# Performance work log

Measured on AMD Instinct MI355X. Metric: run time of the kernel, lower is better.

Reference implementation:

```python
import jax, jax.numpy as jnp
import numpy as np

# RPE constants from the source: pix_per_patch=200//16, alpha=12, beta=24, gamma=96, num_buckets=49
ALPHA, BETA, GAMMA, PPP = 12.0, 24.0, 96.0, 12.0
NUM_BUCKETS = 49
LN_EPS = 1e-5


def _layernorm(x, w, b):
    m = jnp.mean(x, axis=-1, keepdims=True)
    v = jnp.mean((x - m) ** 2, axis=-1, keepdims=True)
    return (x - m) / jnp.sqrt(v + LN_EPS) * w + b


def _bucket_ids(ct):
    # ct: (B,T,2) int coords -> piecewise_index bucket ids shifted by beta, (B,T,T) int32
    ctf = ct.astype(jnp.float32)
    diff = ctf[:, :, None, :] - ctf[:, None, :, :]          # (B,T,T,2)
    dist = jnp.sqrt(jnp.sum(diff * diff, axis=-1))           # euclidean distance
    rel = jnp.trunc(dist / PPP)                              # torch.div(..., rounding_mode='trunc')
    abs_r = jnp.abs(rel)
    log_branch = jnp.sign(rel) * jnp.minimum(
        jnp.round(ALPHA + jnp.log(jnp.maximum(abs_r, 1e-6) / ALPHA) / np.log(GAMMA / ALPHA) * (BETA - ALPHA)),
        BETA)
    idx = jnp.where(abs_r <= ALPHA, jnp.round(rel), log_branch).astype(jnp.int32)
    return idx + int(BETA)                                   # shift into [0, num_buckets)


def setup_inputs() -> dict:
    key = jax.random.key(0)
    ks = jax.random.split(key, 12)
    B, T, C, H = 32, 500, 512, 8
    s = 0.02
    return {
        "x": jax.random.normal(ks[0], (B, T, C), jnp.float32),
        "ct": jax.random.randint(ks[1], (B, T, 2), 0, 200, jnp.int32),
        "w_attn": jax.random.normal(ks[2], (C, 3 * C), jnp.float32) * s,
        "b_attn": jnp.zeros((3 * C,), jnp.float32),
        "w_proj": jax.random.normal(ks[3], (C, C), jnp.float32) * s,
        "b_proj": jnp.zeros((C,), jnp.float32),
        "rpe_table": jax.random.normal(ks[4], (H, NUM_BUCKETS), jnp.float32) * s,
        "ln1_w": jnp.ones((C,), jnp.float32),
        "ln1_b": jnp.zeros((C,), jnp.float32),
        "ln2_w": jnp.ones((C,), jnp.float32),
        "ln2_b": jnp.zeros((C,), jnp.float32),
        "w_fc": jax.random.normal(ks[5], (C, 2 * C), jnp.float32) * s,
        "b_fc": jnp.zeros((2 * C,), jnp.float32),
        "w_fc2": jax.random.normal(ks[6], (2 * C, C), jnp.float32) * s,
        "b_fc2": jnp.zeros((C,), jnp.float32),
    }


def reference(x, ct, w_attn, b_attn, w_proj, b_proj, rpe_table,
              ln1_w, ln1_b, ln2_w, ln2_b, w_fc, b_fc, w_fc2, b_fc2):
    B, T, C = x.shape
    H = rpe_table.shape[0]
    D = C // H

    # --- RPEAttention ---
    bucket = _bucket_ids(ct)                                  # (B,T,T) int32 in [0,49)
    qkv = x @ w_attn + b_attn                                 # (B,T,3C)
    q, k, v = jnp.split(qkv, 3, axis=-1)
    q = q.reshape(B, T, H, D).transpose(0, 2, 1, 3)           # (B,H,T,D)
    k = k.reshape(B, T, H, D).transpose(0, 2, 1, 3)
    v = v.reshape(B, T, H, D).transpose(0, 2, 1, 3)
    att = jnp.einsum('bhtd,bhsd->bhts', q, k) * (1.0 / np.sqrt(D))
    # bias buffer is all ones -> masked_fill(bias==0) is a no-op
    # faithful replication of torch: table[:, flat].view(B,H,T,T) (a raw reshape of (H, B*T*T))
    rpe = rpe_table[:, bucket.reshape(-1)].reshape(B, H, T, T)
    att = jax.nn.softmax(att + rpe, axis=-1)
    y = jnp.einsum('bhts,bhsd->bthd', att, v).reshape(B, T, C)
    y = y @ w_proj + b_proj

    # --- Block: residual + LN, MLP (GELU exact), residual + LN ---
    x = _layernorm(x + y, ln1_w, ln1_b)
    h = jax.nn.gelu(x @ w_fc + b_fc, approximate=False)
    x = _layernorm(x + (h @ w_fc2 + b_fc2), ln2_w, ln2_b)
    return x
```

## Files before the change

### kernel.cpp

```cpp
#include <hip/hip_runtime.h>
#include <cstdint>
#include <cstddef>


typedef unsigned short ushort_t;
typedef __bf16 bf16x8 __attribute__((ext_vector_type(8)));
typedef float floatx4 __attribute__((ext_vector_type(4)));
typedef unsigned short ushort4v __attribute__((ext_vector_type(4)));
typedef unsigned short ushort8v __attribute__((ext_vector_type(8)));

#define DEV __device__ __forceinline__

#define B_ 32
#define T_ 500
#define C_ 512
#define H_ 8
#define M_ 16000

#define OFF_QK     0ULL
#define OFF_XBF    32800768ULL
#define OFF_BUCKET 49184768ULL
#define OFF_VT     57376768ULL
#define OFF_Y      74153984ULL
#define OFF_WATTN  90537984ULL
#define OFF_WPROJ  92110848ULL
#define OFF_WFC    92635136ULL
#define OFF_WFC2   93683712ULL
#define VT_BYTES   16777216ULL

DEV ushort_t f2bf(float f) {
  union { float f; unsigned u; } v; v.f = f;
  unsigned r = v.u + 0x7fffu + ((v.u >> 16) & 1u);
  return (ushort_t)(r >> 16);
}
DEV float bf2f(ushort_t u) {
  union { unsigned u; float f; } v; v.u = ((unsigned)u) << 16;
  return v.f;
}

DEV void gload16(const void* g, void* l) {
  __builtin_amdgcn_global_load_lds(
      (__attribute__((address_space(1))) void*)(g),
      (__attribute__((address_space(3))) void*)(l), 16, 0, 0);
}

__global__ __launch_bounds__(256) void cvt_bf16(const float* __restrict__ in,
                                                ushort_t* __restrict__ out, int n) {
  int i = (blockIdx.x * 256 + threadIdx.x) * 4;
  if (i >= n) return;
  float4 v = *(const float4*)(in + i);
  ushort4v o = { f2bf(v.x), f2bf(v.y), f2bf(v.z), f2bf(v.w) };
  *(ushort4v*)(out + i) = o;
}

struct WTDesc { const float* w; ushort_t* wt; int K; int N; };
struct WTArgs { WTDesc d[4]; };

__global__ __launch_bounds__(256) void wtrans_all(WTArgs a) {
  const int bid = blockIdx.x;
  int z, local;
  if (bid < 768)       { z = 0; local = bid; }
  else if (bid < 1024) { z = 1; local = bid - 768; }
  else if (bid < 1536) { z = 2; local = bid - 1024; }
  else                 { z = 3; local = bid - 1536; }
  const WTDesc dd = a.d[z];
  const int gx = dd.N >> 5;
  const int n0 = (local % gx) * 32, k0 = (local / gx) * 32;

  __shared__ float tile[32][33];
  const int c = threadIdx.x & 31, r = threadIdx.x >> 5;
#pragma unroll
  for (int rr = 0; rr < 4; ++rr)
    tile[r + rr * 8][c] = dd.w[(size_t)(k0 + r + rr * 8) * dd.N + n0 + c];
  __syncthreads();
#pragma unroll
  for (int rr = 0; rr < 4; ++rr)
    dd.wt[(size_t)(n0 + r + rr * 8) * dd.K + k0 + c] = f2bf(tile[c][r + rr * 8]);
}

__global__ __launch_bounds__(256) void bucket_kernel(const int* __restrict__ ct,
                                                     unsigned char* __restrict__ bucket) {
  const int b = blockIdx.y;
  const int tid = threadIdx.x, w = tid >> 6, lane = tid & 63;
  __shared__ int2 ctS[500];
  for (int j = tid; j < T_; j += 256) ctS[j] = ((const int2*)ct)[(size_t)b * T_ + j];
  __syncthreads();
  const int t = blockIdx.x * 4 + w;
  const int2 a = ctS[t];
  const float ax = (float)a.x, ay = (float)a.y;
  const size_t rowbase = (size_t)(b * T_ + t) << 9;
#pragma unroll
  for (int it = 0; it < 8; ++it) {
    const int s = it * 64 + lane;
    if (s < T_) {
      const int2 c2 = ctS[s];
      const float dx = ax - (float)c2.x, dy = ay - (float)c2.y;
      const float dist = sqrtf(dx * dx + dy * dy);
      const float rel = truncf(dist / 12.0f);
      const float far = fminf(rintf(12.0f + logf(rel / 12.0f) * (12.0f / 2.0794415416798357f)), 24.0f);
      const float idx = (rel <= 12.0f) ? rel : far;
      bucket[rowbase + (s >> 6) * 64 + (s & 15) * 4 + ((s >> 4) & 3)]
          = (unsigned char)((int)idx + 24);
    }
  }
}

__global__ __launch_bounds__(256, 2)
void gemm_qkv(const ushort_t* __restrict__ A,
              const ushort_t* __restrict__ Bt,
              const float* __restrict__ bias,
              ushort_t* __restrict__ qk,
              ushort_t* __restrict__ vt) {
  constexpr int K = 512;
  const int bid = blockIdx.x;
  const int xcd = bid & 7, k = bid >> 3;
  const int n_blk = k % 12, mg = k / 12;
  const int m_blk = mg * 8 + xcd;
  if (m_blk >= 125) return;
  const int m0 = m_blk * 128, n0 = n_blk * 128;

  __shared__ __align__(16) ushort_t As[128 * 64];
  __shared__ __align__(16) ushort_t Bs[128 * 64];
  const int tid = threadIdx.x;
  const int lane = tid & 63, w = tid >> 6;
  const int wm = w >> 1, wn = w & 1;
  const int quad = lane >> 4, l15 = lane & 15;

  floatx4 acc[4][4] = {};

  for (int k0 = 0; k0 < K; k0 += 64) {
    __syncthreads();
#pragma unroll
    for (int j = 0; j < 4; ++j) {
      const int chunk = j * 256 + tid;
      const int row = chunk >> 3, pos = chunk & 7, c = pos ^ (row & 7);
      gload16(A + (size_t)(m0 + row) * K + k0 + c * 8, (char*)As + j * 4096 + w * 1024);
      gload16(Bt + (size_t)(n0 + row) * K + k0 + c * 8, (char*)Bs + j * 4096 + w * 1024);
    }
    asm volatile("s_waitcnt vmcnt(0)" ::: "memory");
    __syncthreads();

#pragma unroll
    for (int kq = 0; kq < 2; ++kq) {
      bf16x8 af[4], bfr[4];
#pragma unroll
      for (int t = 0; t < 4; ++t) {
        const int rowa = wm * 64 + t * 16 + l15;
        const int posa = (kq * 4 + quad) ^ (rowa & 7);
        af[t] = *(const bf16x8*)((const char*)As + rowa * 128 + posa * 16);
        const int rowb = wn * 64 + t * 16 + l15;
        const int posb = (kq * 4 + quad) ^ (rowb & 7);
        bfr[t] = *(const bf16x8*)((const char*)Bs + rowb * 128 + posb * 16);
      }
#pragma unroll
      for (int tm = 0; tm < 4; ++tm)
#pragma unroll
        for (int tn = 0; tn < 4; ++tn)
          acc[tm][tn] = __builtin_amdgcn_mfma_f32_16x16x32_bf16(af[tm], bfr[tn], acc[tm][tn], 0, 0, 0);
    }
  }

  if (n0 < 1024) {
#pragma unroll
    for (int tn = 0; tn < 4; ++tn) {
      const int n = n0 + wn * 64 + tn * 16 + l15;
      const float bs = bias[n];
#pragma unroll
      for (int tm = 0; tm < 4; ++tm)
#pragma unroll
        for (int r = 0; r < 4; ++r) {
          const int m = m0 + wm * 64 + tm * 16 + quad * 4 + r;
          qk[(size_t)m * 1024 + n] = f2bf(acc[tm][tn][r] + bs);
        }
    }
  } else {
#pragma unroll
    for (int tn = 0; tn < 4; ++tn) {
      const int n = n0 + wn * 64 + tn * 16 + l15;
      const float bs = bias[n];
      const int hh = (n >> 6) - 16, dd = n & 63;
#pragma unroll
      for (int tm = 0; tm < 4; ++tm) {
        const int mb = m0 + wm * 64 + tm * 16 + quad * 4;
        const int bb = mb / 500;
        const int ss = mb - bb * 500;
        ushort4v pk;
#pragma unroll
        for (int r = 0; r < 4; ++r) pk[r] = f2bf(acc[tm][tn][r] + bs);
        *(ushort4v*)(vt + (((size_t)(bb * 8 + hh)) * 64 + dd) * 512 + ss) = pk;
      }
    }
  }
}

template <int TN, int EPI>
__global__ __launch_bounds__(256, TN == 64 ? 4 : 2)
void gemm_bt(const ushort_t* __restrict__ A,
             const ushort_t* __restrict__ Bt,
             const float* __restrict__ bias,
             const float* __restrict__ resf,
             const ushort_t* __restrict__ resb,
             void* __restrict__ outp,
             int N, int K) {
  constexpr int TMW = (TN == 128) ? 4 : 2;
  const int nn = N / TN;
  const int bid = blockIdx.x;
  const int xcd = bid & 7, kk = bid >> 3;
  const int n_blk = kk % nn, mg = kk / nn;
  const int m_blk = mg * 8 + xcd;
  if (m_blk >= 125) return;
  const int m0 = m_blk * 128, n0 = n_blk * TN;

  __shared__ __align__(16) ushort_t As[128 * 64];
  __shared__ __align__(16) ushort_t Bs[TN * 64];
  const int tid = threadIdx.x;
  const int lane = tid & 63, w = tid >> 6;
  const int wm = (TN == 128) ? (w >> 1) : w;
  const int wn = (TN == 128) ? (w & 1) : 0;
  const int quad = lane >> 4, l15 = lane & 15;

  floatx4 acc[TMW][4] = {};

  for (int k0 = 0; k0 < K; k0 += 64) {
    __syncthreads();
#pragma unroll
    for (int j = 0; j < 4; ++j) {
      const int chunk = j * 256 + tid;
      const int row = chunk >> 3, pos = chunk & 7, c = pos ^ (row & 7);
      gload16(A + (size_t)(m0 + row) * K + k0 + c * 8, (char*)As + j * 4096 + w * 1024);
    }
#pragma unroll
    for (int j = 0; j < TN / 32; ++j) {
      const int chunk = j * 256 + tid;
      const int row = chunk >> 3, pos = chunk & 7, c = pos ^ (row & 7);
      gload16(Bt + (size_t)(n0 + row) * K + k0 + c * 8, (char*)Bs + j * 4096 + w * 1024);
    }
    asm volatile("s_waitcnt vmcnt(0)" ::: "memory");
    __syncthreads();

#pragma unroll
    for (int kq = 0; kq < 2; ++kq) {
      bf16x8 af[TMW], bfr[4];
#pragma unroll
      for (int t = 0; t < TMW; ++t) {
        const int row = wm * (TMW * 16) + t * 16 + l15;
        const int pos = (kq * 4 + quad) ^ (row & 7);
        af[t] = *(const bf16x8*)((const char*)As + row * 128 + pos * 16);
      }
#pragma unroll
      for (int t = 0; t < 4; ++t) {
        const int row = wn * 64 + t * 16 + l15;
        const int pos = (kq * 4 + quad) ^ (row & 7);
        bfr[t] = *(const bf16x8*)((const char*)Bs + row * 128 + pos * 16);
      }
#pragma unroll
      for (int tm = 0; tm < TMW; ++tm)
#pragma unroll
        for (int tn = 0; tn < 4; ++tn)
          acc[tm][tn] = __builtin_amdgcn_mfma_f32_16x16x32_bf16(af[tm], bfr[tn], acc[tm][tn], 0, 0, 0);
    }
  }

#pragma unroll
  for (int tn = 0; tn < 4; ++tn) {
    const int n = n0 + wn * 64 + tn * 16 + l15;
    const float bs = bias[n];
#pragma unroll
    for (int tm = 0; tm < TMW; ++tm) {
#pragma unroll
      for (int r = 0; r < 4; ++r) {
        const int m = m0 + wm * (TMW * 16) + tm * 16 + quad * 4 + r;
        const float v = acc[tm][tn][r] + bs;
        if (EPI == 1) {
          const float gv = 0.5f * v * (1.0f + erff(v * 0.70710678118654752f));
          ((ushort_t*)outp)[(size_t)m * N + n] = f2bf(gv);
        } else if (EPI == 2) {
          ((float*)outp)[(size_t)m * N + n] = v + resf[(size_t)m * N + n];
        } else {
          ((float*)outp)[(size_t)m * N + n] = v + bf2f(resb[(size_t)m * N + n]);
        }
      }
    }
  }
}

__global__ __launch_bounds__(256, 5) void attn_kernel(const ushort_t* __restrict__ qk,
                                                      const ushort_t* __restrict__ vt,
                                                      const unsigned char* __restrict__ bucket,
                                                      const float* __restrict__ rpe,
                                                      ushort_t* __restrict__ y) {
  const int bid = blockIdx.x;
  const int xcd = bid & 7, sl = bid >> 3;
  const int qt = sl & 7;
  const int pair = xcd * 32 + (sl >> 3);
  const int h = pair >> 5, b = pair & 31;
  const int g = b >> 2;
  const int bpp = 8 * (b & 3) + h;

  __shared__ __align__(16) ushort_t Qs[64 * 64];
  __shared__ __align__(16) ushort_t Ks[64 * 64];
  __shared__ __align__(16) ushort_t VTs[64 * 64];
  __shared__ float tbl2[224];

  const int tid = threadIdx.x;
  const int lane = tid & 63, w = tid >> 6;
  const int quad = lane >> 4, l15 = lane & 15;
  const int t0 = qt * 64;

#pragma unroll
  for (int j = 0; j < 2; ++j) {
    const int chunk = j * 256 + tid;
    const int row = chunk >> 3, pos = chunk & 7, c = pos ^ (row & 7);
    gload16(qk + (size_t)(b * T_ + t0 + row) * 1024 + h * 64 + c * 8,
            (char*)Qs + j * 4096 + w * 1024);
  }
  if (tid < 224) {
    const int q = tid / 52, i = tid - q * 52;
    tbl2[tid] = (q < 4 && i < 49) ? rpe[g * 49 + i] * 1.44269504f : 0.0f;
  }
  asm volatile("s_waitcnt vmcnt(0)" ::: "memory");
  __syncthreads();

  bf16x8 qf[2];
#pragma unroll
  for (int kq = 0; kq < 2; ++kq) {
    const int row = w * 16 + l15;
    const int pos = (kq * 4 + quad) ^ (row & 7);
    qf[kq] = *(const bf16x8*)((const char*)Qs + row * 128 + pos * 16);
  }

  floatx4 o[4] = {};
  float lsum[4] = {0.0f, 0.0f, 0.0f, 0.0f};
  char* pw = (char*)Qs + w * 2048;

  const unsigned char* bkbase[4];
#pragma unroll
  for (int r = 0; r < 4; ++r) {
    const int tr = t0 + w * 16 + quad * 4 + r;
    const int trc = (tr < T_) ? tr : (T_ - 1);
    bkbase[r] = bucket + ((size_t)(bpp * T_ + trc) << 9) + (l15 << 2);
  }

  for (int st = 0; st < 8; ++st) {
    const int s0 = st * 64;
    __syncthreads();
#pragma unroll
    for (int j = 0; j < 2; ++j) {
      const int chunk = j * 256 + tid;
      const int row = chunk >> 3, pos = chunk & 7, c = pos ^ (row & 7);
      gload16(qk + (size_t)(b * T_ + s0 + row) * 1024 + 512 + h * 64 + c * 8,
              (char*)Ks + j * 4096 + w * 1024);
      gload16(vt + ((size_t)(b * 8 + h) * 64 + row) * 512 + s0 + c * 8,
              (char*)VTs + j * 4096 + w * 1024);
    }
    unsigned bw[4];
#pragma unroll
    for (int r = 0; r < 4; ++r) bw[r] = *(const unsigned*)(bkbase[r] + s0);
    asm volatile("s_waitcnt vmcnt(0)" ::: "memory");
    __syncthreads();

    floatx4 sc[4];
#pragma unroll
    for (int tn = 0; tn < 4; ++tn) {
      floatx4 z = {0.0f, 0.0f, 0.0f, 0.0f};
#pragma unroll
      for (int kq = 0; kq < 2; ++kq) {
        const int row = tn * 16 + l15;
        const int pos = (kq * 4 + quad) ^ (row & 7);
        const bf16x8 kf = *(const bf16x8*)((const char*)Ks + row * 128 + pos * 16);
        z = __builtin_amdgcn_mfma_f32_16x16x32_bf16(qf[kq], kf, z, 0, 0, 0);
      }
      sc[tn] = z;
    }

#pragma unroll
    for (int r = 0; r < 4; ++r) {
      const int prow = quad * 4 + r;
#pragma unroll
      for (int tn = 0; tn < 4; ++tn) {
        const int scol = s0 + tn * 16 + l15;
        const int idx = (bw[r] >> (tn * 8)) & 63;
        const float val = fmaf(sc[tn][r], 0.18033688f, tbl2[quad * 52 + idx]);
        const float p = (scol < T_) ? exp2f(val) : 0.0f;
        lsum[r] += p;
        const int chunk = (tn * 2 + (l15 >> 3)) ^ (prow & 7);
        *(ushort_t*)(pw + prow * 128 + chunk * 16 + (l15 & 7) * 2) =
            (ushort_t)(__builtin_bit_cast(unsigned, p) >> 16);
      }
    }
    asm volatile("" ::: "memory");

#pragma unroll
    for (int ks = 0; ks < 2; ++ks) {
      const int ppos = (ks * 4 + quad) ^ (l15 & 7);
      const bf16x8 pf = *(const bf16x8*)(pw + l15 * 128 + ppos * 16);
#pragma unroll
      for (int nd = 0; nd < 4; ++nd) {
        const int row = nd * 16 + l15;
        const int pos = (ks * 4 + quad) ^ (row & 7);
        const bf16x8 vf = *(const bf16x8*)((const char*)VTs + row * 128 + pos * 16);
        o[nd] = __builtin_amdgcn_mfma_f32_16x16x32_bf16(pf, vf, o[nd], 0, 0, 0);
      }
    }
  }

#pragma unroll
  for (int r = 0; r < 4; ++r) {
    float s = lsum[r];
    s += __shfl_xor(s, 1);
    s += __shfl_xor(s, 2);
    s += __shfl_xor(s, 4);
    s += __shfl_xor(s, 8);
    const int t = t0 + w * 16 + quad * 4 + r;
    if (t < T_) {
      const float inv = 1.0f / s;
#pragma unroll
      for (int nd = 0; nd < 4; ++nd)
        y[((size_t)b * T_ + t) * 512 + h * 64 + nd * 16 + l15] = f2bf(o[nd][r] * inv);
    }
  }
}

__global__ __launch_bounds__(256) void ln_kernel(const float* z,
                                                 const float* __restrict__ gw,
                                                 const float* __restrict__ gb,
                                                 ushort_t* out_bf, float* out_f) {
  const int row = blockIdx.x;
  const int tid = threadIdx.x, lane = tid & 63, w = tid >> 6;
  const float* zr = z + (size_t)row * 512;
  const float2 v = *(const float2*)(zr + tid * 2);
  float s = v.x + v.y;
#pragma unroll
  for (int m = 1; m < 64; m <<= 1) s += __shfl_xor(s, m);
  __shared__ float red[8];
  if (lane == 0) red[w] = s;
  __syncthreads();
  const float mean = (red[0] + red[1] + red[2] + red[3]) * (1.0f / 512.0f);
  const float d0 = v.x - mean, d1 = v.y - mean;
  float q = d0 * d0 + d1 * d1;
#pragma unroll
  for (int m = 1; m < 64; m <<= 1) q += __shfl_xor(q, m);
  if (lane == 0) red[4 + w] = q;
  __syncthreads();
  const float var = (red[4] + red[5] + red[6] + red[7]) * (1.0f / 512.0f);
  const float rstd = rsqrtf(var + 1e-5f);
  const int c0 = tid * 2;
  const float o0 = d0 * rstd * gw[c0] + gb[c0];
  const float o1 = d1 * rstd * gw[c0 + 1] + gb[c0 + 1];
  if (out_bf) {
    out_bf[(size_t)row * 512 + c0] = f2bf(o0);
    out_bf[(size_t)row * 512 + c0 + 1] = f2bf(o1);
  }
  if (out_f) {
    float2 ov; ov.x = o0; ov.y = o1;
    *(float2*)(out_f + (size_t)row * 512 + c0) = ov;
  }
}

extern "C" void kernel_launch(void* const* d_in, const int* in_sizes, int n_in,
                              void* d_out, int out_size, void* d_ws, size_t ws_size,
                              hipStream_t stream) {
  (void)in_sizes; (void)n_in; (void)out_size; (void)ws_size;
  const float* x      = (const float*)d_in[0];
  const int*   ct     = (const int*)d_in[1];
  const float* w_attn = (const float*)d_in[2];
  const float* b_attn = (const float*)d_in[3];
  const float* w_proj = (const float*)d_in[4];
  const float* b_proj = (const float*)d_in[5];
  const float* rpe    = (const float*)d_in[6];
  const float* ln1w   = (const float*)d_in[7];
  const float* ln1b   = (const float*)d_in[8];
  const float* ln2w   = (const float*)d_in[9];
  const float* ln2b   = (const float*)d_in[10];
  const float* w_fc   = (const float*)d_in[11];
  const float* b_fc   = (const float*)d_in[12];
  const float* w_fc2  = (const float*)d_in[13];
  const float* b_fc2  = (const float*)d_in[14];
  float* out = (float*)d_out;

  char* ws = (char*)d_ws;
  ushort_t* qk      = (ushort_t*)(ws + OFF_QK);
  ushort_t* h_buf   = (ushort_t*)(ws + OFF_QK);
  ushort_t* x_bf    = (ushort_t*)(ws + OFF_XBF);
  ushort_t* x1      = (ushort_t*)(ws + OFF_XBF);
  unsigned char* bk = (unsigned char*)(ws + OFF_BUCKET);
  ushort_t* vt      = (ushort_t*)(ws + OFF_VT);
  ushort_t* y       = (ushort_t*)(ws + OFF_Y);
  ushort_t* wt_attn = (ushort_t*)(ws + OFF_WATTN);
  ushort_t* wt_proj = (ushort_t*)(ws + OFF_WPROJ);
  ushort_t* wt_fc   = (ushort_t*)(ws + OFF_WFC);
  ushort_t* wt_fc2  = (ushort_t*)(ws + OFF_WFC2);

  cvt_bf16<<<dim3(8000), 256, 0, stream>>>(x, x_bf, M_ * C_);
  WTArgs wta;
  wta.d[0] = { w_attn, wt_attn, 512, 1536 };
  wta.d[1] = { w_proj, wt_proj, 512, 512 };
  wta.d[2] = { w_fc,   wt_fc,   512, 1024 };
  wta.d[3] = { w_fc2,  wt_fc2,  1024, 512 };
  wtrans_all<<<dim3(2048), 256, 0, stream>>>(wta);
  bucket_kernel<<<dim3(125, 32), 256, 0, stream>>>(ct, bk);
  hipMemsetAsync(vt, 0, VT_BYTES, stream);

  gemm_qkv<<<dim3(1536), 256, 0, stream>>>(x_bf, wt_attn, b_attn, qk, vt);
  attn_kernel<<<dim3(2048), 256, 0, stream>>>(qk, vt, bk, rpe, y);
  gemm_bt<64, 2><<<dim3(1024), 256, 0, stream>>>(y, wt_proj, b_proj, x, nullptr, out, 512, 512);
  ln_kernel<<<dim3(16000), 256, 0, stream>>>(out, ln1w, ln1b, x1, nullptr);
  gemm_bt<128, 1><<<dim3(1024), 256, 0, stream>>>(x1, wt_fc, b_fc, nullptr, nullptr, h_buf, 1024, 512);
  gemm_bt<64, 3><<<dim3(1024), 256, 0, stream>>>(h_buf, wt_fc2, b_fc2, nullptr, x1, out, 512, 1024);
  ln_kernel<<<dim3(16000), 256, 0, stream>>>(out, ln2w, ln2b, nullptr, out);
}
```

Measured before the change: 327.4 us.

## Prefetch K/V tiles in attention, use bpermute for RPE table, warp-per-row layernorm

The attention kernel now keeps K and V fragments in registers and prefetches the next 64-column tile from global memory into LDS while computing the current one. This hides the load latency that was previously exposed each iteration. It replaces the LDS RPE table with a per-lane register read through ds_bpermute, raises wave priority around the MFMAs, and masks only on the last tile. The bucket kernel uses fast hardware sqrt/log intrinsics, and layernorm processes one row per wavefront with vectorized loads and no LDS reduction. Risks are higher register pressure at occupancy 5 and small accuracy differences from the approximate sqrt/log near bucket boundaries.

```diff
diff --git a/kernel.cpp b/kernel.cpp
--- a/kernel.cpp
+++ b/kernel.cpp
@@ -95,9 +95,10 @@
     if (s < T_) {
       const int2 c2 = ctS[s];
       const float dx = ax - (float)c2.x, dy = ay - (float)c2.y;
-      const float dist = sqrtf(dx * dx + dy * dy);
-      const float rel = truncf(dist / 12.0f);
-      const float far = fminf(rintf(12.0f + logf(rel / 12.0f) * (12.0f / 2.0794415416798357f)), 24.0f);
+      const float dist = __builtin_amdgcn_sqrtf(dx * dx + dy * dy);
+      const float rel = truncf(dist * (1.0f / 12.0f));
+      const float far = fminf(
+          rintf(fmaf(__builtin_amdgcn_logf(rel * (1.0f / 12.0f)), 4.0f, 12.0f)), 24.0f);
       const float idx = (rel <= 12.0f) ? rel : far;
       bucket[rowbase + (s >> 6) * 64 + (s & 15) * 4 + ((s >> 4) & 3)]
           = (unsigned char)((int)idx + 24);
@@ -300,7 +301,6 @@
   __shared__ __align__(16) ushort_t Qs[64 * 64];
   __shared__ __align__(16) ushort_t Ks[64 * 64];
   __shared__ __align__(16) ushort_t VTs[64 * 64];
-  __shared__ float tbl2[224];
 
   const int tid = threadIdx.x;
   const int lane = tid & 63, w = tid >> 6;
@@ -313,11 +313,25 @@
     const int row = chunk >> 3, pos = chunk & 7, c = pos ^ (row & 7);
     gload16(qk + (size_t)(b * T_ + t0 + row) * 1024 + h * 64 + c * 8,
             (char*)Qs + j * 4096 + w * 1024);
-  }
-  if (tid < 224) {
-    const int q = tid / 52, i = tid - q * 52;
-    tbl2[tid] = (q < 4 && i < 49) ? rpe[g * 49 + i] * 1.44269504f : 0.0f;
-  }
+    gload16(qk + (size_t)(b * T_ + row) * 1024 + 512 + h * 64 + c * 8,
+            (char*)Ks + j * 4096 + w * 1024);
+    gload16(vt + ((size_t)(b * 8 + h) * 64 + row) * 512 + c * 8,
+            (char*)VTs + j * 4096 + w * 1024);
+  }
+
+  const float treg = rpe[g * 49 + (lane < 49 ? lane : 48)] * 1.44269504f;
+
+  const unsigned char* bkbase[4];
+#pragma unroll
+  for (int r = 0; r < 4; ++r) {
+    const int tr = t0 + w * 16 + quad * 4 + r;
+    const int trc = (tr < T_) ? tr : (T_ - 1);
+    bkbase[r] = bucket + ((size_t)(bpp * T_ + trc) << 9) + (l15 << 2);
+  }
+  unsigned bw[4];
+#pragma unroll
+  for (int r = 0; r < 4; ++r) bw[r] = *(const unsigned*)(bkbase[r]);
+
   asm volatile("s_waitcnt vmcnt(0)" ::: "memory");
   __syncthreads();
 
@@ -329,59 +343,60 @@
     qf[kq] = *(const bf16x8*)((const char*)Qs + row * 128 + pos * 16);
   }
 
+  bf16x8 kreg[8], vreg[8];
+#pragma unroll
+  for (int kq = 0; kq < 2; ++kq)
+#pragma unroll
+    for (int tn = 0; tn < 4; ++tn) {
+      const int row = tn * 16 + l15;
+      const int pos = (kq * 4 + quad) ^ (row & 7);
+      kreg[kq * 4 + tn] = *(const bf16x8*)((const char*)Ks + row * 128 + pos * 16);
+      vreg[kq * 4 + tn] = *(const bf16x8*)((const char*)VTs + row * 128 + pos * 16);
+    }
+
   floatx4 o[4] = {};
   float lsum[4] = {0.0f, 0.0f, 0.0f, 0.0f};
   char* pw = (char*)Qs + w * 2048;
 
-  const unsigned char* bkbase[4];
-#pragma unroll
-  for (int r = 0; r < 4; ++r) {
-    const int tr = t0 + w * 16 + quad * 4 + r;
-    const int trc = (tr < T_) ? tr : (T_ - 1);
-    bkbase[r] = bucket + ((size_t)(bpp * T_ + trc) << 9) + (l15 << 2);
-  }
-
-  for (int st = 0; st < 8; ++st) {
-    const int s0 = st * 64;
+  auto tile = [&](int s0, bool last) {
     __syncthreads();
-#pragma unroll
-    for (int j = 0; j < 2; ++j) {
-      const int chunk = j * 256 + tid;
-      const int row = chunk >> 3, pos = chunk & 7, c = pos ^ (row & 7);
-      gload16(qk + (size_t)(b * T_ + s0 + row) * 1024 + 512 + h * 64 + c * 8,
-              (char*)Ks + j * 4096 + w * 1024);
-      gload16(vt + ((size_t)(b * 8 + h) * 64 + row) * 512 + s0 + c * 8,
-              (char*)VTs + j * 4096 + w * 1024);
-    }
-    unsigned bw[4];
-#pragma unroll
-    for (int r = 0; r < 4; ++r) bw[r] = *(const unsigned*)(bkbase[r] + s0);
-    asm volatile("s_waitcnt vmcnt(0)" ::: "memory");
-    __syncthreads();
+    unsigned bwn[4];
+    if (!last) {
+      const int s0n = s0 + 64;
+#pragma unroll
+      for (int j = 0; j < 2; ++j) {
+        const int chunk = j * 256 + tid;
+        const int row = chunk >> 3, pos = chunk & 7, c = pos ^ (row & 7);
+        gload16(qk + (size_t)(b * T_ + s0n + row) * 1024 + 512 + h * 64 + c * 8,
+                (char*)Ks + j * 4096 + w * 1024);
+        gload16(vt + ((size_t)(b * 8 + h) * 64 + row) * 512 + s0n + c * 8,
+                (char*)VTs + j * 4096 + w * 1024);
+      }
+#pragma unroll
+      for (int r = 0; r < 4; ++r) bwn[r] = *(const unsigned*)(bkbase[r] + s0n);
+    }
 
     floatx4 sc[4];
+    __builtin_amdgcn_s_setprio(1);
 #pragma unroll
     for (int tn = 0; tn < 4; ++tn) {
       floatx4 z = {0.0f, 0.0f, 0.0f, 0.0f};
-#pragma unroll
-      for (int kq = 0; kq < 2; ++kq) {
-        const int row = tn * 16 + l15;
-        const int pos = (kq * 4 + quad) ^ (row & 7);
-        const bf16x8 kf = *(const bf16x8*)((const char*)Ks + row * 128 + pos * 16);
-        z = __builtin_amdgcn_mfma_f32_16x16x32_bf16(qf[kq], kf, z, 0, 0, 0);
-      }
+      z = __builtin_amdgcn_mfma_f32_16x16x32_bf16(qf[0], kreg[tn], z, 0, 0, 0);
+      z = __builtin_amdgcn_mfma_f32_16x16x32_bf16(qf[1], kreg[4 + tn], z, 0, 0, 0);
       sc[tn] = z;
     }
+    __builtin_amdgcn_s_setprio(0);
 
 #pragma unroll
     for (int r = 0; r < 4; ++r) {
       const int prow = quad * 4 + r;
 #pragma unroll
       for (int tn = 0; tn < 4; ++tn) {
-        const int scol = s0 + tn * 16 + l15;
-        const int idx = (bw[r] >> (tn * 8)) & 63;
-        const float val = fmaf(sc[tn][r], 0.18033688f, tbl2[quad * 52 + idx]);
-        const float p = (scol < T_) ? exp2f(val) : 0.0f;
+        const int idx4 = (int)((bw[r] >> (tn * 8)) & 63u) * 4;
+        const float tv = __builtin_bit_cast(float,
+            __builtin_amdgcn_ds_bpermute(idx4, __builtin_bit_cast(int, treg)));
+        float p = __builtin_amdgcn_exp2f(fmaf(sc[tn][r], 0.18033688f, tv));
+        if (last && (tn * 16 + l15 >= 52)) p = 0.0f;
         lsum[r] += p;
         const int chunk = (tn * 2 + (l15 >> 3)) ^ (prow & 7);
         *(ushort_t*)(pw + prow * 128 + chunk * 16 + (l15 & 7) * 2) =
@@ -390,19 +405,37 @@
     }
     asm volatile("" ::: "memory");
 
+    __builtin_amdgcn_s_setprio(1);
 #pragma unroll
     for (int ks = 0; ks < 2; ++ks) {
       const int ppos = (ks * 4 + quad) ^ (l15 & 7);
-      const bf16x8 pf = *(const bf16x8*)(pw + l15 * 128 + ppos * 16);
-#pragma unroll
-      for (int nd = 0; nd < 4; ++nd) {
-        const int row = nd * 16 + l15;
-        const int pos = (ks * 4 + quad) ^ (row & 7);
-        const bf16x8 vf = *(const bf16x8*)((const char*)VTs + row * 128 + pos * 16);
-        o[nd] = __builtin_amdgcn_mfma_f32_16x16x32_bf16(pf, vf, o[nd], 0, 0, 0);
-      }
-    }
-  }
+      const bf16x8 pfr = *(const bf16x8*)(pw + l15 * 128 + ppos * 16);
+#pragma unroll
+      for (int nd = 0; nd < 4; ++nd)
+        o[nd] = __builtin_amdgcn_mfma_f32_16x16x32_bf16(pfr, vreg[ks * 4 + nd], o[nd], 0, 0, 0);
+    }
+    __builtin_amdgcn_s_setprio(0);
+
+    if (!last) {
+      asm volatile("s_waitcnt vmcnt(0)" ::: "memory");
+      __syncthreads();
+#pragma unroll
+      for (int kq = 0; kq < 2; ++kq)
+#pragma unroll
+        for (int tn = 0; tn < 4; ++tn) {
+          const int row = tn * 16 + l15;
+          const int pos = (kq * 4 + quad) ^ (row & 7);
+          kreg[kq * 4 + tn] = *(const bf16x8*)((const char*)Ks + row * 128 + pos * 16);
+          vreg[kq * 4 + tn] = *(const bf16x8*)((const char*)VTs + row * 128 + pos * 16);
+        }
+#pragma unroll
+      for (int r = 0; r < 4; ++r) bw[r] = bwn[r];
+    }
+  };
+
+#pragma unroll 1
+  for (int st = 0; st < 7; ++st) tile(st * 64, false);
+  tile(448, true);
 
 #pragma unroll
   for (int r = 0; r < 4; ++r) {
@@ -425,35 +458,48 @@
                                                  const float* __restrict__ gw,
                                                  const float* __restrict__ gb,
                                                  ushort_t* out_bf, float* out_f) {
-  const int row = blockIdx.x;
   const int tid = threadIdx.x, lane = tid & 63, w = tid >> 6;
+  const int row = blockIdx.x * 4 + w;
   const float* zr = z + (size_t)row * 512;
-  const float2 v = *(const float2*)(zr + tid * 2);
-  float s = v.x + v.y;
+  const int c0 = lane * 8;
+  const float4 v0 = *(const float4*)(zr + c0);
+  const float4 v1 = *(const float4*)(zr + c0 + 4);
+  float s = ((v0.x + v0.y) + (v0.z + v0.w)) + ((v1.x + v1.y) + (v1.z + v1.w));
 #pragma unroll
   for (int m = 1; m < 64; m <<= 1) s += __shfl_xor(s, m);
-  __shared__ float red[8];
-  if (lane == 0) red[w] = s;
-  __syncthreads();
-  const float mean = (red[0] + red[1] + red[2] + red[3]) * (1.0f / 512.0f);
-  const float d0 = v.x - mean, d1 = v.y - mean;
-  float q = d0 * d0 + d1 * d1;
+  const float mean = s * (1.0f / 512.0f);
+  float d[8] = { v0.x - mean, v0.y - mean, v0.z - mean, v0.w - mean,
+                 v1.x - mean, v1.y - mean, v1.z - mean, v1.w - mean };
+  float q = 0.0f;
+#pragma unroll
+  for (int j = 0; j < 8; ++j) q += d[j] * d[j];
 #pragma unroll
   for (int m = 1; m < 64; m <<= 1) q += __shfl_xor(q, m);
-  if (lane == 0) red[4 + w] = q;
-  __syncthreads();
-  const float var = (red[4] + red[5] + red[6] + red[7]) * (1.0f / 512.0f);
-  const float rstd = rsqrtf(var + 1e-5f);
-  const int c0 = tid * 2;
-  const float o0 = d0 * rstd * gw[c0] + gb[c0];
-  const float o1 = d1 * rstd * gw[c0 + 1] + gb[c0 + 1];
+  const float rstd = rsqrtf(q * (1.0f / 512.0f) + 1e-5f);
+  const float4 ga = *(const float4*)(gw + c0);
+  const float4 gc = *(const float4*)(gw + c0 + 4);
+  const float4 ba = *(const float4*)(gb + c0);
+  const float4 bc = *(const float4*)(gb + c0 + 4);
+  float ov[8];
+  ov[0] = d[0] * rstd * ga.x + ba.x;
+  ov[1] = d[1] * rstd * ga.y + ba.y;
+  ov[2] = d[2] * rstd * ga.z + ba.z;
+  ov[3] = d[3] * rstd * ga.w + ba.w;
+  ov[4] = d[4] * rstd * gc.x + bc.x;
+  ov[5] = d[5] * rstd * gc.y + bc.y;
+  ov[6] = d[6] * rstd * gc.z + bc.z;
+  ov[7] = d[7] * rstd * gc.w + bc.w;
   if (out_bf) {
-    out_bf[(size_t)row * 512 + c0] = f2bf(o0);
-    out_bf[(size_t)row * 512 + c0 + 1] = f2bf(o1);
+    ushort8v pk;
+#pragma unroll
+    for (int j = 0; j < 8; ++j) pk[j] = f2bf(ov[j]);
+    *(ushort8v*)(out_bf + (size_t)row * 512 + c0) = pk;
   }
   if (out_f) {
-    float2 ov; ov.x = o0; ov.y = o1;
-    *(float2*)(out_f + (size_t)row * 512 + c0) = ov;
+    float4 o0 = { ov[0], ov[1], ov[2], ov[3] };
+    float4 o1 = { ov[4], ov[5], ov[6], ov[7] };
+    *(float4*)(out_f + (size_t)row * 512 + c0) = o0;
+    *(float4*)(out_f + (size_t)row * 512 + c0 + 4) = o1;
   }
 }
 
@@ -504,8 +550,8 @@
   gemm_qkv<<<dim3(1536), 256, 0, stream>>>(x_bf, wt_attn, b_attn, qk, vt);
   attn_kernel<<<dim3(2048), 256, 0, stream>>>(qk, vt, bk, rpe, y);
   gemm_bt<64, 2><<<dim3(1024), 256, 0, stream>>>(y, wt_proj, b_proj, x, nullptr, out, 512, 512);
-  ln_kernel<<<dim3(16000), 256, 0, stream>>>(out, ln1w, ln1b, x1, nullptr);
+  ln_kernel<<<dim3(4000), 256, 0, stream>>>(out, ln1w, ln1b, x1, nullptr);
   gemm_bt<128, 1><<<dim3(1024), 256, 0, stream>>>(x1, wt_fc, b_fc, nullptr, nullptr, h_buf, 1024, 512);
   gemm_bt<64, 3><<<dim3(1024), 256, 0, stream>>>(h_buf, wt_fc2, b_fc2, nullptr, x1, out, 512, 1024);
-  ln_kernel<<<dim3(16000), 256, 0, stream>>>(out, ln2w, ln2b, nullptr, out);
-}
+  ln_kernel<<<dim3(4000), 256, 0, stream>>>(out, ln2w, ln2b, nullptr, out);
+}
```

New measurement: 510.5 us. +55.9%, slower.
